# Optimization experiments

Hardware: AMD Instinct MI355X
Metric: run time of the kernel (lower is better)

## Reference

```python
import jax, jax.numpy as jnp
import numpy as np

B, IN_DIM, HID, PROJ, OUT = 32768, 4097, 2048, 512, 3
FEAT = IN_DIM - 1
EPS = 1e-12  # F.normalize eps


def setup_inputs() -> dict:
    key = jax.random.key(0)
    ks = jax.random.split(key, 16)
    x_feat = jax.random.normal(ks[0], (B, FEAT), dtype=jnp.float32)
    flag = jax.random.randint(ks[1], (B, 1), 0, 2).astype(jnp.float32)
    x = jnp.concatenate([x_feat, flag], axis=1)  # [B, IN_DIM], last col is 0/1 flag

    def lin(k, fan_in, fan_out):
        bound = 1.0 / np.sqrt(fan_in)
        kw, kb = jax.random.split(k)
        W = jax.random.uniform(kw, (fan_in, fan_out), jnp.float32, -bound, bound)
        b = jax.random.uniform(kb, (fan_out,), jnp.float32, -bound, bound)
        return W, b

    W1n, b1n = lin(ks[2], FEAT, HID)
    W2n, b2n = lin(ks[3], HID, PROJ)
    Wcn, bcn = lin(ks[4], PROJ, OUT)
    W1o, b1o = lin(ks[5], FEAT, HID)
    W2o, b2o = lin(ks[6], HID, PROJ)
    Wco, bco = lin(ks[7], PROJ, OUT)
    return {"x": x, "W1n": W1n, "b1n": b1n, "W2n": W2n, "b2n": b2n,
            "Wcn": Wcn, "bcn": bcn, "W1o": W1o, "b1o": b1o, "W2o": W2o,
            "b2o": b2o, "Wco": Wco, "bco": bco}


def _path(feat, W1, b1, W2, b2):
    # Linear -> ReLU -> Dropout(eval: identity) -> Linear
    h = jax.nn.relu(feat @ W1 + b1)
    return h @ W2 + b2  # [B, PROJ]


def reference(x, W1n, b1n, W2n, b2n, Wcn, bcn, W1o, b1o, W2o, b2o, Wco, bco):
    flag = x[:, -1:] > 0.5          # [B,1] bool; 1 -> natural path
    feat = x[:, :-1]                # [B, FEAT]
    # Dense 2-expert compute + select (same math as gather/scatter routing).
    z_nat = _path(feat, W1n, b1n, W2n, b2n)
    z_oth = _path(feat, W1o, b1o, W2o, b2o)
    z = jnp.where(flag, z_nat, z_oth)                      # [B, PROJ]
    logits_nat = jax.nn.relu(z_nat) @ Wcn + bcn
    logits_oth = jax.nn.relu(z_oth) @ Wco + bco
    logits = jnp.where(flag, logits_nat, logits_oth)       # [B, OUT]
    norm = jnp.linalg.norm(z, axis=1, keepdims=True)
    z_normalized = z / jnp.maximum(norm, EPS)
    return (z_normalized, logits)
```

## Files before the change

kernel.cpp:

```cpp
#include <hip/hip_runtime.h>
#include <hip/hip_bf16.h>

typedef __bf16 bf16_t;
typedef __attribute__((ext_vector_type(8))) __bf16 bf16x8;
typedef __attribute__((ext_vector_type(4))) __bf16 bf16x4;
typedef __attribute__((ext_vector_type(4))) float f32x4;

#define NROWS 32768
#define FEAT  4096
#define INDIM 4097
#define HID   2048
#define PROJ  512
#define NPAD  33024
#define MT256 129
#define SENT  0xFFFFFFFFu

__device__ __forceinline__ void load_lds16(const bf16_t* g, char* s) {
  __builtin_amdgcn_global_load_lds(
      (__attribute__((address_space(1))) void*)(void*)g,
      (__attribute__((address_space(3))) void*)s, 16, 0, 0);
}

__global__ __launch_bounds__(256) void init_kernel(unsigned* __restrict__ perm,
                                                   int* __restrict__ cnt) {
  int i = blockIdx.x * 256 + threadIdx.x;
  if (i < NPAD) perm[i] = SENT;
  if (i < 4) cnt[i] = 0;
}

__global__ __launch_bounds__(256) void count_kernel(const float* __restrict__ x,
                                                    int* __restrict__ cnt) {
  int i = blockIdx.x * 256 + threadIdx.x;
  if (i >= NROWS) return;
  float f = x[(long)i * INDIM + FEAT];
  if (f > 0.5f) atomicAdd(&cnt[0], 1);
}

__global__ __launch_bounds__(256) void scatter_kernel(const float* __restrict__ x,
                                                      unsigned* __restrict__ perm,
                                                      int* __restrict__ cnt) {
  int i = blockIdx.x * 256 + threadIdx.x;
  if (i >= NROWS) return;
  float f = x[(long)i * INDIM + FEAT];
  int g = (f > 0.5f) ? 0 : 1;
  int pos = atomicAdd(&cnt[1 + g], 1);
  int off_oth = ((cnt[0] + 255) >> 8) << 8;
  int q = (g == 0) ? pos : off_oth + pos;
  perm[q] = (unsigned)i;
}

__global__ __launch_bounds__(256) void convert_x_kernel(const float* __restrict__ x,
                                                        bf16_t* __restrict__ xbf) {
  const int lane = threadIdx.x & 63;
  const long wid = ((long)blockIdx.x * 256 + threadIdx.x) >> 6;
  const long chunk = wid * 512;
  const long row = chunk >> 12;
  const long col = chunk & 4095;
  const float* src = x + row * INDIM + col + lane;
  bf16_t* dst = xbf + chunk + lane;
#pragma unroll
  for (int j = 0; j < 8; ++j)
    dst[j * 64] = (bf16_t)src[j * 64];
}

__global__ __launch_bounds__(256) void transpose_convert_kernel(
    const float* __restrict__ W, bf16_t* __restrict__ Wt, int K, int N) {
  __shared__ float tile[32][33];
  const int n0 = blockIdx.x << 5;
  const int k0 = blockIdx.y << 5;
  const int t = threadIdx.x;
  const int r = t >> 3;
  const int c4 = (t & 7) << 2;
  f32x4 v = *(const f32x4*)(W + (long)(k0 + r) * N + n0 + c4);
#pragma unroll
  for (int i = 0; i < 4; ++i) tile[r][c4 + i] = v[i];
  __syncthreads();
  bf16x4 o;
#pragma unroll
  for (int i = 0; i < 4; ++i) o[i] = (bf16_t)tile[c4 + i][r];
  *(bf16x4*)(Wt + (long)(n0 + r) * K + k0 + c4) = o;
}

template <bool GATHER, bool RELU_BF16>
__global__ __launch_bounds__(512, 2) void gemm256_kernel(
    const bf16_t* __restrict__ A,
    const bf16_t* __restrict__ BtNat, const bf16_t* __restrict__ BtOth,
    const float* __restrict__ biasNat, const float* __restrict__ biasOth,
    void* __restrict__ Cout,
    const unsigned* __restrict__ perm, const int* __restrict__ cnt,
    const int K, const int N, const int ntn) {
  extern __shared__ char smem[];
  const int tid = threadIdx.x;

  const int nwg = gridDim.x;
  const int q8 = nwg >> 3, r8g = nwg & 7;
  const int xcd = blockIdx.x & 7, lo = blockIdx.x >> 3;
  const int wg = (xcd < r8g ? xcd * (q8 + 1) : r8g * (q8 + 1) + (xcd - r8g) * q8) + lo;
  const int tile_m = wg / ntn;
  const int tile_n = wg - tile_m * ntn;
  const int qbase = tile_m << 8;
  if (perm[qbase] == SENT) return;
  const int n0 = tile_n << 8;

  const int off_oth = ((cnt[0] + 255) >> 8) << 8;
  const bool nat = qbase < off_oth;
  const bf16_t* __restrict__ Bt = nat ? BtNat : BtOth;
  const float* __restrict__ bias = nat ? biasNat : biasOth;

  const int nkt = K >> 6;
  const int niter = K >> 7;

  const int r8 = tid >> 3;
  const int kco = ((tid & 7) ^ (r8 & 7)) << 3;
  long r00, r01, r10, r11;
  if (GATHER) {
    unsigned p00 = perm[qbase + r8];
    unsigned p10 = perm[qbase + 64 + r8];
    unsigned p01 = perm[qbase + 128 + r8];
    unsigned p11 = perm[qbase + 192 + r8];
    r00 = (p00 == SENT) ? 0 : (long)p00;
    r10 = (p10 == SENT) ? 0 : (long)p10;
    r01 = (p01 == SENT) ? 0 : (long)p01;
    r11 = (p11 == SENT) ? 0 : (long)p11;
  } else {
    r00 = qbase + r8;       r10 = qbase + 64 + r8;
    r01 = qbase + 128 + r8; r11 = qbase + 192 + r8;
  }
  const bf16_t* aS00 = A + r00 * K + kco;
  const bf16_t* aS10 = A + r10 * K + kco;
  const bf16_t* aS01 = A + r01 * K + kco;
  const bf16_t* aS11 = A + r11 * K + kco;

  const int b0 = tid >> 8;
  const int r32 = r8 & 31;
  const bf16_t* bS00 = Bt + (long)(n0 + b0 * 64 + r32) * K + kco;
  const bf16_t* bS10 = Bt + (long)(n0 + b0 * 64 + 32 + r32) * K + kco;
  const bf16_t* bS01 = Bt + (long)(n0 + 128 + b0 * 64 + r32) * K + kco;
  const bf16_t* bS11 = Bt + (long)(n0 + 128 + b0 * 64 + 32 + r32) * K + kco;

  const int wave = tid >> 6, lane = tid & 63;
  const int wmi = wave >> 2, wni = wave & 3;
  const int quad = lane >> 4, l16 = lane & 15;
  const int x7 = l16 & 7;
  const int rx0 = (quad ^ x7) << 4;
  const int rx1 = ((quad + 4) ^ x7) << 4;
  const int aRB = (wmi * 64 + l16) * 128;
  const int bRB = (wni * 32 + l16) * 128;
  const int wbase = wave << 10;

#define ADST(buf, h, j) ((buf) * 32768 + (h) * 16384 + (j) * 8192)
#define BDST(buf, h, j) (65536 + (buf) * 32768 + (h) * 16384 + (j) * 8192)
#define STG_A(buf, h, kt) do { const long ko = ((kt) < nkt) ? ((long)(kt) << 6) : 0; \
    load_lds16(aS##h##0 + ko, smem + ADST(buf, h, 0) + wbase); \
    load_lds16(aS##h##1 + ko, smem + ADST(buf, h, 1) + wbase); } while (0)
#define STG_B(buf, h, kt) do { const long ko = ((kt) < nkt) ? ((long)(kt) << 6) : 0; \
    load_lds16(bS##h##0 + ko, smem + BDST(buf, h, 0) + wbase); \
    load_lds16(bS##h##1 + ko, smem + BDST(buf, h, 1) + wbase); } while (0)
#define RD_A(buf, mi, ks) af[(mi) & 3][ks] = *(const bf16x8*)(smem + (buf) * 32768 \
    + ((mi) >> 2) * 16384 + aRB + ((mi) & 3) * 2048 + rx##ks)
#define RD_B(buf, nf, ks) bfr[nf][ks] = *(const bf16x8*)(smem + 65536 + (buf) * 32768 \
    + ((nf) >> 1) * 16384 + bRB + ((nf) & 1) * 2048 + rx##ks)
#define MFMA_PH(m0_, n0_) do { \
    __builtin_amdgcn_s_setprio(1); \
    _Pragma("unroll") for (int ks_ = 0; ks_ < 2; ++ks_) \
    _Pragma("unroll") for (int mi_ = 0; mi_ < 4; ++mi_) \
    _Pragma("unroll") for (int ni_ = 0; ni_ < 2; ++ni_) \
      acc[(m0_) + mi_][(n0_) + ni_] = __builtin_amdgcn_mfma_f32_16x16x32_bf16( \
          af[mi_][ks_], bfr[(n0_) + ni_][ks_], acc[(m0_) + mi_][(n0_) + ni_], 0, 0, 0); \
    __builtin_amdgcn_s_setprio(0); } while (0)
#define SBAR do { __builtin_amdgcn_sched_barrier(0); __builtin_amdgcn_s_barrier(); } while (0)
#define VMC6 asm volatile("s_waitcnt vmcnt(6)" ::: "memory")

  f32x4 acc[8][4] = {};
  bf16x8 af[4][2], bfr[4][2];

  STG_A(0, 0, 0); STG_B(0, 0, 0); STG_B(0, 1, 0); STG_A(0, 1, 0);
  STG_A(1, 0, 1); STG_B(1, 0, 1); STG_B(1, 1, 1);
  VMC6; SBAR;

  for (int t = 0; t < niter; ++t) {
    const int c = t << 1;
    RD_A(0, 0, 0); RD_A(0, 0, 1); RD_A(0, 1, 0); RD_A(0, 1, 1);
    RD_A(0, 2, 0); RD_A(0, 2, 1); RD_A(0, 3, 0); RD_A(0, 3, 1);
    RD_B(0, 0, 0); RD_B(0, 0, 1); RD_B(0, 1, 0); RD_B(0, 1, 1);
    STG_A(1, 1, c + 1);
    SBAR;
    MFMA_PH(0, 0);
    SBAR;
    RD_B(0, 2, 0); RD_B(0, 2, 1); RD_B(0, 3, 0); RD_B(0, 3, 1);
    STG_A(0, 0, c + 2);
    SBAR;
    MFMA_PH(0, 2);
    SBAR;
    RD_A(0, 4, 0); RD_A(0, 4, 1); RD_A(0, 5, 0); RD_A(0, 5, 1);
    RD_A(0, 6, 0); RD_A(0, 6, 1); RD_A(0, 7, 0); RD_A(0, 7, 1);
    STG_B(0, 0, c + 2);
    SBAR;
    MFMA_PH(4, 0);
    SBAR;
    STG_B(0, 1, c + 2);
    SBAR;
    MFMA_PH(4, 2);
    VMC6;
    SBAR;
    RD_A(1, 0, 0); RD_A(1, 0, 1); RD_A(1, 1, 0); RD_A(1, 1, 1);
    RD_A(1, 2, 0); RD_A(1, 2, 1); RD_A(1, 3, 0); RD_A(1, 3, 1);
    RD_B(1, 0, 0); RD_B(1, 0, 1); RD_B(1, 1, 0); RD_B(1, 1, 1);
    STG_A(0, 1, c + 2);
    SBAR;
    MFMA_PH(0, 0);
    SBAR;
    RD_B(1, 2, 0); RD_B(1, 2, 1); RD_B(1, 3, 0); RD_B(1, 3, 1);
    STG_A(1, 0, c + 3);
    SBAR;
    MFMA_PH(0, 2);
    SBAR;
    RD_A(1, 4, 0); RD_A(1, 4, 1); RD_A(1, 5, 0); RD_A(1, 5, 1);
    RD_A(1, 6, 0); RD_A(1, 6, 1); RD_A(1, 7, 0); RD_A(1, 7, 1);
    STG_B(1, 0, c + 3);
    SBAR;
    MFMA_PH(4, 0);
    SBAR;
    STG_B(1, 1, c + 3);
    SBAR;
    MFMA_PH(4, 2);
    VMC6;
    SBAR;
  }

  asm volatile("s_waitcnt vmcnt(0)" ::: "memory");

  float bv[4];
#pragma unroll
  for (int nf = 0; nf < 4; ++nf) bv[nf] = bias[n0 + wni * 64 + nf * 16 + l16];

#pragma unroll
  for (int mi = 0; mi < 8; ++mi) {
    const long row0 = (long)(qbase + wmi * 128 + mi * 16 + quad * 4);
#pragma unroll
    for (int nf = 0; nf < 4; ++nf) {
      const int col = n0 + wni * 64 + nf * 16 + l16;
#pragma unroll
      for (int r = 0; r < 4; ++r) {
        float v = acc[mi][nf][r] + bv[nf];
        if (RELU_BF16) {
          v = fmaxf(v, 0.0f);
          ((bf16_t*)Cout)[(row0 + r) * N + col] = (bf16_t)v;
        } else {
          ((float*)Cout)[(row0 + r) * N + col] = v;
        }
      }
    }
  }
#undef ADST
#undef BDST
#undef STG_A
#undef STG_B
#undef RD_A
#undef RD_B
#undef MFMA_PH
#undef SBAR
#undef VMC6
}

__global__ __launch_bounds__(256) void epilogue_kernel(
    const float* __restrict__ z,
    const float* __restrict__ Wc0, const float* __restrict__ bc0,
    const float* __restrict__ Wc1, const float* __restrict__ bc1,
    const unsigned* __restrict__ perm, const int* __restrict__ cnt,
    float* __restrict__ out_z, float* __restrict__ out_logits) {
  __shared__ float WcL[2][PROJ * 3];
  for (int i = threadIdx.x; i < PROJ * 3; i += 256) {
    WcL[0][i] = Wc0[i];
    WcL[1][i] = Wc1[i];
  }
  __syncthreads();
  const int wave = threadIdx.x >> 6;
  const int lane = threadIdx.x & 63;
  const int q = blockIdx.x * 4 + wave;
  const unsigned orig = perm[q];
  if (orig == SENT) return;
  const int n_nat = cnt[0];
  const int off_oth = ((n_nat + 255) >> 8) << 8;
  const int g = (q < off_oth) ? 0 : 1;

  float zv[8];
  float ss = 0.f, l0 = 0.f, l1 = 0.f, l2 = 0.f;
#pragma unroll
  for (int i = 0; i < 8; ++i) {
    const int k = i * 64 + lane;
    float v = z[(long)q * PROJ + k];
    zv[i] = v;
    ss += v * v;
    float r = fmaxf(v, 0.f);
    const float* w = &WcL[g][k * 3];
    l0 += r * w[0];
    l1 += r * w[1];
    l2 += r * w[2];
  }
#pragma unroll
  for (int off = 32; off > 0; off >>= 1) {
    ss += __shfl_xor(ss, off);
    l0 += __shfl_xor(l0, off);
    l1 += __shfl_xor(l1, off);
    l2 += __shfl_xor(l2, off);
  }
  const float inv = 1.f / fmaxf(sqrtf(ss), 1e-12f);
#pragma unroll
  for (int i = 0; i < 8; ++i)
    out_z[(long)orig * PROJ + i * 64 + lane] = zv[i] * inv;
  if (lane == 0) {
    const float* bc = g ? bc1 : bc0;
    out_logits[(long)orig * 3 + 0] = l0 + bc[0];
    out_logits[(long)orig * 3 + 1] = l1 + bc[1];
    out_logits[(long)orig * 3 + 2] = l2 + bc[2];
  }
}

extern "C" void kernel_launch(void* const* d_in, const int* in_sizes, int n_in,
                              void* d_out, int out_size, void* d_ws, size_t ws_size,
                              hipStream_t stream) {
  const float* x   = (const float*)d_in[0];
  const float* W1n = (const float*)d_in[1];
  const float* b1n = (const float*)d_in[2];
  const float* W2n = (const float*)d_in[3];
  const float* b2n = (const float*)d_in[4];
  const float* Wcn = (const float*)d_in[5];
  const float* bcn = (const float*)d_in[6];
  const float* W1o = (const float*)d_in[7];
  const float* b1o = (const float*)d_in[8];
  const float* W2o = (const float*)d_in[9];
  const float* b2o = (const float*)d_in[10];
  const float* Wco = (const float*)d_in[11];
  const float* bco = (const float*)d_in[12];

  char* ws = (char*)d_ws;
  bf16_t* xbf  = (bf16_t*)ws;
  float*  z_ws = (float*)ws;
  size_t off = 268435456;
  bf16_t* W1tn = (bf16_t*)(ws + off); off += (size_t)FEAT * HID * 2;
  bf16_t* W1to = (bf16_t*)(ws + off); off += (size_t)FEAT * HID * 2;
  bf16_t* W2tn = (bf16_t*)(ws + off); off += (size_t)HID * PROJ * 2;
  bf16_t* W2to = (bf16_t*)(ws + off); off += (size_t)HID * PROJ * 2;
  bf16_t* h_ws = (bf16_t*)(ws + off); off += (size_t)NPAD * HID * 2;
  unsigned* perm = (unsigned*)(ws + off); off += (size_t)NPAD * 4;
  int* cnt = (int*)(ws + off);

  float* out_z = (float*)d_out;
  float* out_logits = out_z + (size_t)NROWS * PROJ;

  static bool attr_done = false;
  if (!attr_done) {
    auto* k1 = gemm256_kernel<true, true>;
    auto* k2 = gemm256_kernel<false, false>;
    (void)hipFuncSetAttribute(reinterpret_cast<const void*>(k1),
                              hipFuncAttributeMaxDynamicSharedMemorySize, 131072);
    (void)hipFuncSetAttribute(reinterpret_cast<const void*>(k2),
                              hipFuncAttributeMaxDynamicSharedMemorySize, 131072);
    attr_done = true;
  }

  init_kernel<<<(NPAD + 255) / 256, 256, 0, stream>>>(perm, cnt);
  count_kernel<<<NROWS / 256, 256, 0, stream>>>(x, cnt);
  scatter_kernel<<<NROWS / 256, 256, 0, stream>>>(x, perm, cnt);

  convert_x_kernel<<<(int)(((long)NROWS * FEAT / 512) / 4), 256, 0, stream>>>(x, xbf);
  transpose_convert_kernel<<<dim3(HID / 32, FEAT / 32), 256, 0, stream>>>(W1n, W1tn, FEAT, HID);
  transpose_convert_kernel<<<dim3(HID / 32, FEAT / 32), 256, 0, stream>>>(W1o, W1to, FEAT, HID);
  transpose_convert_kernel<<<dim3(PROJ / 32, HID / 32), 256, 0, stream>>>(W2n, W2tn, HID, PROJ);
  transpose_convert_kernel<<<dim3(PROJ / 32, HID / 32), 256, 0, stream>>>(W2o, W2to, HID, PROJ);

  gemm256_kernel<true, true><<<dim3(MT256 * 8), 512, 131072, stream>>>(
      xbf, W1tn, W1to, b1n, b1o, (void*)h_ws, perm, cnt, FEAT, HID, 8);

  gemm256_kernel<false, false><<<dim3(MT256 * 2), 512, 131072, stream>>>(
      h_ws, W2tn, W2to, b2n, b2o, (void*)z_ws, perm, cnt, HID, PROJ, 2);

  epilogue_kernel<<<NPAD / 4, 256, 0, stream>>>(
      z_ws, Wcn, bcn, Wco, bco, perm, cnt, out_z, out_logits);
}
```

Measured before the change: 1.726 ms.

## Restructure GEMM prefetch schedule, drop intra-phase barriers, vectorize x conversion

The GEMM main loop now issues the whole next-stage prefetch earlier, with A and B staged in pairs and the last A half staged in the prologue. It replaces the barrier before each MFMA phase with a plain scheduling barrier and raises the vmcnt wait threshold to match the extra loads in flight. The intent is fewer workgroup barriers and more memory/compute overlap. This relies on careful buffer-reuse ordering, and a reordering mistake could corrupt LDS contents. Separately, the x conversion kernel becomes a grid-stride loop over 2048 blocks that writes 8 bf16 values per thread as one vector store, but reads fp32 unaligned per element.

New measurement: 1.696 ms. About the same (-1.7%).

```diff
diff --git a/kernel.cpp b/kernel.cpp
--- a/kernel.cpp
+++ b/kernel.cpp
@@ -51,16 +51,18 @@
 
 __global__ __launch_bounds__(256) void convert_x_kernel(const float* __restrict__ x,
                                                         bf16_t* __restrict__ xbf) {
-  const int lane = threadIdx.x & 63;
-  const long wid = ((long)blockIdx.x * 256 + threadIdx.x) >> 6;
-  const long chunk = wid * 512;
-  const long row = chunk >> 12;
-  const long col = chunk & 4095;
-  const float* src = x + row * INDIM + col + lane;
-  bf16_t* dst = xbf + chunk + lane;
-#pragma unroll
-  for (int j = 0; j < 8; ++j)
-    dst[j * 64] = (bf16_t)src[j * 64];
+  const long total = (long)NROWS * FEAT / 8;
+  const long stride = (long)gridDim.x * 256;
+  for (long u = (long)blockIdx.x * 256 + threadIdx.x; u < total; u += stride) {
+    const long e = u << 3;
+    const long row = e >> 12;
+    const long col = e & 4095;
+    const float* s = x + row * INDIM + col;
+    bf16x8 o;
+#pragma unroll
+    for (int j = 0; j < 8; ++j) o[j] = (bf16_t)s[j];
+    *(bf16x8*)(xbf + e) = o;
+  }
 }
 
 __global__ __launch_bounds__(256) void transpose_convert_kernel(
@@ -168,63 +170,62 @@
       acc[(m0_) + mi_][(n0_) + ni_] = __builtin_amdgcn_mfma_f32_16x16x32_bf16( \
           af[mi_][ks_], bfr[(n0_) + ni_][ks_], acc[(m0_) + mi_][(n0_) + ni_], 0, 0, 0); \
     __builtin_amdgcn_s_setprio(0); } while (0)
+#define SCHED0 __builtin_amdgcn_sched_barrier(0)
 #define SBAR do { __builtin_amdgcn_sched_barrier(0); __builtin_amdgcn_s_barrier(); } while (0)
-#define VMC6 asm volatile("s_waitcnt vmcnt(6)" ::: "memory")
+#define VMC8 asm volatile("s_waitcnt vmcnt(8)" ::: "memory")
 
   f32x4 acc[8][4] = {};
   bf16x8 af[4][2], bfr[4][2];
 
   STG_A(0, 0, 0); STG_B(0, 0, 0); STG_B(0, 1, 0); STG_A(0, 1, 0);
-  STG_A(1, 0, 1); STG_B(1, 0, 1); STG_B(1, 1, 1);
-  VMC6; SBAR;
+  STG_A(1, 0, 1); STG_B(1, 0, 1); STG_B(1, 1, 1); STG_A(1, 1, 1);
+  VMC8; SBAR;
 
   for (int t = 0; t < niter; ++t) {
     const int c = t << 1;
     RD_A(0, 0, 0); RD_A(0, 0, 1); RD_A(0, 1, 0); RD_A(0, 1, 1);
     RD_A(0, 2, 0); RD_A(0, 2, 1); RD_A(0, 3, 0); RD_A(0, 3, 1);
     RD_B(0, 0, 0); RD_B(0, 0, 1); RD_B(0, 1, 0); RD_B(0, 1, 1);
-    STG_A(1, 1, c + 1);
-    SBAR;
+    SCHED0;
     MFMA_PH(0, 0);
     SBAR;
     RD_B(0, 2, 0); RD_B(0, 2, 1); RD_B(0, 3, 0); RD_B(0, 3, 1);
-    STG_A(0, 0, c + 2);
-    SBAR;
+    STG_A(0, 0, c + 2); STG_B(0, 0, c + 2);
+    SCHED0;
     MFMA_PH(0, 2);
     SBAR;
     RD_A(0, 4, 0); RD_A(0, 4, 1); RD_A(0, 5, 0); RD_A(0, 5, 1);
     RD_A(0, 6, 0); RD_A(0, 6, 1); RD_A(0, 7, 0); RD_A(0, 7, 1);
-    STG_B(0, 0, c + 2);
-    SBAR;
+    STG_B(0, 1, c + 2);
+    SCHED0;
     MFMA_PH(4, 0);
     SBAR;
-    STG_B(0, 1, c + 2);
-    SBAR;
+    STG_A(0, 1, c + 2);
+    SCHED0;
     MFMA_PH(4, 2);
-    VMC6;
+    VMC8;
     SBAR;
     RD_A(1, 0, 0); RD_A(1, 0, 1); RD_A(1, 1, 0); RD_A(1, 1, 1);
     RD_A(1, 2, 0); RD_A(1, 2, 1); RD_A(1, 3, 0); RD_A(1, 3, 1);
     RD_B(1, 0, 0); RD_B(1, 0, 1); RD_B(1, 1, 0); RD_B(1, 1, 1);
-    STG_A(0, 1, c + 2);
-    SBAR;
+    SCHED0;
     MFMA_PH(0, 0);
     SBAR;
     RD_B(1, 2, 0); RD_B(1, 2, 1); RD_B(1, 3, 0); RD_B(1, 3, 1);
-    STG_A(1, 0, c + 3);
-    SBAR;
+    STG_A(1, 0, c + 3); STG_B(1, 0, c + 3);
+    SCHED0;
     MFMA_PH(0, 2);
     SBAR;
     RD_A(1, 4, 0); RD_A(1, 4, 1); RD_A(1, 5, 0); RD_A(1, 5, 1);
     RD_A(1, 6, 0); RD_A(1, 6, 1); RD_A(1, 7, 0); RD_A(1, 7, 1);
-    STG_B(1, 0, c + 3);
-    SBAR;
+    STG_B(1, 1, c + 3);
+    SCHED0;
     MFMA_PH(4, 0);
     SBAR;
-    STG_B(1, 1, c + 3);
-    SBAR;
+    STG_A(1, 1, c + 3);
+    SCHED0;
     MFMA_PH(4, 2);
-    VMC6;
+    VMC8;
     SBAR;
   }
 
@@ -259,8 +260,9 @@
 #undef RD_A
 #undef RD_B
 #undef MFMA_PH
+#undef SCHED0
 #undef SBAR
-#undef VMC6
+#undef VMC8
 }
 
 __global__ __launch_bounds__(256) void epilogue_kernel(
@@ -364,7 +366,7 @@
   count_kernel<<<NROWS / 256, 256, 0, stream>>>(x, cnt);
   scatter_kernel<<<NROWS / 256, 256, 0, stream>>>(x, perm, cnt);
 
-  convert_x_kernel<<<(int)(((long)NROWS * FEAT / 512) / 4), 256, 0, stream>>>(x, xbf);
+  convert_x_kernel<<<2048, 256, 0, stream>>>(x, xbf);
   transpose_convert_kernel<<<dim3(HID / 32, FEAT / 32), 256, 0, stream>>>(W1n, W1tn, FEAT, HID);
   transpose_convert_kernel<<<dim3(HID / 32, FEAT / 32), 256, 0, stream>>>(W1o, W1to, FEAT, HID);
   transpose_convert_kernel<<<dim3(PROJ / 32, HID / 32), 256, 0, stream>>>(W2n, W2tn, HID, PROJ);
```
